# Optimization experiments

Hardware: AMD Instinct MI355X
Metric: run time of the kernel (lower is better)

Reference implementation:

```python
import jax, jax.numpy as jnp
import numpy as np

N = 8192
NFEAT = 512
NHID = 256
NCLASS = 128


def setup_inputs() -> dict:
    key = jax.random.key(0)
    k1, k2, k3, k4 = jax.random.split(key, 4)
    feature_s = jax.random.normal(k1, (N, NFEAT), dtype=jnp.float32)
    feature_t = jax.random.normal(k2, (N, NFEAT), dtype=jnp.float32)
    # nn.Linear(in, out, bias=False) weight has shape [out, in]
    w1 = jax.random.normal(k3, (NHID, NFEAT), dtype=jnp.float32) * (1.0 / np.sqrt(NFEAT))
    w2 = jax.random.normal(k4, (NCLASS, NHID), dtype=jnp.float32) * (1.0 / np.sqrt(NHID))
    return {"feature_s": feature_s, "feature_t": feature_t, "w1": w1, "w2": w2}


def reference(feature_s, feature_t, w1, w2):
    # adj = softmax(feature_s @ feature_t^T) over rows (dim=1)
    adj = jax.nn.softmax(feature_s @ feature_t.T, axis=1)  # [N, N]
    # GCN layer 1: linear(adj @ x) with x = feature_s
    x1 = (adj @ feature_s) @ w1.T  # [N, NHID]
    # GCN layer 2
    x2 = (adj @ x1) @ w2.T  # [N, NCLASS]
    return (x1, x2)
```

## Files before the change

### kernel.cpp

```cpp
#include <hip/hip_runtime.h>
#include <stdint.h>


typedef unsigned short u16;
typedef short bf16x8 __attribute__((ext_vector_type(8)));
typedef _Float16 f16x8 __attribute__((ext_vector_type(8)));
typedef float f32x4 __attribute__((ext_vector_type(4)));

#define EPI_STOREB 0
#define EPI_PARTH  1

__device__ __forceinline__ u16 f2bf(float f) {
  unsigned u = __float_as_uint(f);
  u += 0x7fffu + ((u >> 16) & 1u);
  return (u16)(u >> 16);
}
__device__ __forceinline__ u16 f2h(float f) {
  union { _Float16 h; u16 u; } cv; cv.h = (_Float16)f; return cv.u;
}
__device__ __forceinline__ float h2f(u16 u) {
  union { u16 u; _Float16 h; } cv; cv.u = u; return (float)cv.h;
}
__device__ __forceinline__ int swz8(int r) { return (r ^ (r >> 3)) & 7; }

__device__ __forceinline__ void async16(const void* g, void* lds) {
  __builtin_amdgcn_global_load_lds(
      (const __attribute__((address_space(1))) unsigned int*)g,
      (__attribute__((address_space(3))) unsigned int*)lds, 16, 0, 0);
}

__global__ void probe_layout(int* __restrict__ rmap, int* __restrict__ cmap) {
  const int lane = threadIdx.x & 63;
  const int t = lane & 15, quad = lane >> 4;
  bf16x8 avt, av1;
  const u16 bt = f2bf((float)t), b1 = 0x3f80;
#pragma unroll
  for (int j = 0; j < 8; ++j) { ((u16*)&avt)[j] = bt; ((u16*)&av1)[j] = b1; }
  f32x4 z = {0.f, 0.f, 0.f, 0.f};
  f32x4 r1 = __builtin_amdgcn_mfma_f32_16x16x32_bf16(avt, av1, z, 0, 0, 0);
  f32x4 r2 = __builtin_amdgcn_mfma_f32_16x16x32_bf16(av1, avt, z, 0, 0, 0);
  if (threadIdx.x < 64) {
#pragma unroll
    for (int e = 0; e < 4; ++e) {
      int r = (int)(r1[e] * 0.03125f + 0.5f);
      int c = (int)(r2[e] * 0.03125f + 0.5f);
      if (r < 0 || r > 15) r = quad * 4 + e;
      if (c < 0 || c > 15) c = t;
      rmap[lane * 4 + e] = r;
      cmap[lane * 4 + e] = c;
    }
  }
}

__global__ __launch_bounds__(256) void conv_all(
    const float* __restrict__ Fs, const float* __restrict__ Ft,
    const float* __restrict__ W1, const float* __restrict__ W2,
    u16* __restrict__ Fsf, u16* __restrict__ Ftf,
    u16* __restrict__ W1f, u16* __restrict__ W2h) {
  const int bx = blockIdx.x, tid = threadIdx.x;
  if (bx < 2048) {
    for (int i = bx * 256 + tid; i < 4194304; i += 2048 * 256) Fsf[i] = f2h(Fs[i]);
  } else if (bx < 4096) {
    for (int i = (bx - 2048) * 256 + tid; i < 4194304; i += 2048 * 256) Ftf[i] = f2h(Ft[i]);
  } else if (bx < 4160) {
    for (int i = (bx - 4096) * 256 + tid; i < 131072; i += 64 * 256) W1f[i] = f2h(W1[i]);
  } else {
    for (int i = (bx - 4160) * 256 + tid; i < 32768; i += 16 * 256) W2h[i] = f2bf(W2[i]);
  }
}

__global__ __launch_bounds__(512) void gemm_pexp_f16_256(
    const u16* __restrict__ A, const u16* __restrict__ B, int K, int N,
    u16* __restrict__ P, float* __restrict__ rsp,
    const int* __restrict__ rmap, const int* __restrict__ cmap) {
  __shared__ __align__(16) u16 lA[256 * 64];
  __shared__ __align__(16) u16 lB[128 * 64];
  __shared__ float lrs[256][2];

  const int tid = threadIdx.x;
  const int wave = tid >> 6, lane = tid & 63;
  const int quad = lane >> 4, t = lane & 15;
  const int bm = blockIdx.y * 256, bn = blockIdx.x * 128;
  const int wm = (wave & 3) * 64, wn = (wave >> 2) * 64;

  f32x4 acc[4][4];
#pragma unroll
  for (int i = 0; i < 4; ++i)
#pragma unroll
    for (int j = 0; j < 4; ++j) acc[i][j] = (f32x4){0.f, 0.f, 0.f, 0.f};

  const int srow = tid >> 3, schk = tid & 7;
  const u16* pA[4]; const u16* pB[2];
#pragma unroll
  for (int j = 0; j < 4; ++j) {
    const int r = j * 64 + srow;
    pA[j] = A + (size_t)(bm + r) * K + (schk ^ swz8(r)) * 8;
  }
#pragma unroll
  for (int j = 0; j < 2; ++j) {
    const int r = j * 64 + srow;
    pB[j] = B + (size_t)(bn + r) * K + (schk ^ swz8(r)) * 8;
  }

  int aoffx[4], boffx[4];
#pragma unroll
  for (int i = 0; i < 4; ++i) {
    const int rm = wm + i * 16 + t;
    aoffx[i] = rm * 128 + (swz8(rm) << 4);
    const int rn = wn + i * 16 + t;
    boffx[i] = rn * 128 + (swz8(rn) << 4);
  }
  const int sq0 = quad << 4, sq1 = (quad << 4) | 64;

  for (int k0 = 0; k0 < K; k0 += 64) {
#pragma unroll
    for (int j = 0; j < 4; ++j) {
      async16(pA[j], (char*)lA + j * 8192 + wave * 1024);
      pA[j] += 64;
    }
#pragma unroll
    for (int j = 0; j < 2; ++j) {
      async16(pB[j], (char*)lB + j * 8192 + wave * 1024);
      pB[j] += 64;
    }
    __syncthreads();
#pragma unroll
    for (int s = 0; s < 2; ++s) {
      const int sq = s ? sq1 : sq0;
      f16x8 av[4], bv[4];
#pragma unroll
      for (int i = 0; i < 4; ++i) {
        av[i] = *(const f16x8*)((const char*)lA + (aoffx[i] ^ sq));
        bv[i] = *(const f16x8*)((const char*)lB + (boffx[i] ^ sq));
      }
#pragma unroll
      for (int mi = 0; mi < 4; ++mi)
#pragma unroll
        for (int ni = 0; ni < 4; ++ni)
          acc[mi][ni] = __builtin_amdgcn_mfma_f32_16x16x32_f16(av[mi], bv[ni], acc[mi][ni], 0, 0, 0);
    }
    __syncthreads();
  }

  int rl[4], cl[4];
#pragma unroll
  for (int e = 0; e < 4; ++e) {
    rl[e] = rmap[lane * 4 + e];
    cl[e] = cmap[lane * 4 + e];
  }
#pragma unroll
  for (int mi = 0; mi < 4; ++mi)
#pragma unroll
    for (int e = 0; e < 4; ++e) {
      const int rloc = wm + mi * 16 + rl[e];
      const int row = bm + rloc;
      float s = 0.f;
#pragma unroll
      for (int ni = 0; ni < 4; ++ni) {
        float p = __expf(acc[mi][ni][e] - 100.0f);
        s += p;
        P[(size_t)row * N + (bn + wn + ni * 16 + cl[e])] = f2bf(p);
      }
      s += __shfl_xor(s, 1, 64);
      s += __shfl_xor(s, 2, 64);
      s += __shfl_xor(s, 4, 64);
      s += __shfl_xor(s, 8, 64);
      if (t == 0) lrs[rloc][wave >> 2] = s;
    }
  __syncthreads();
  if (tid < 256)
    rsp[(size_t)blockIdx.x * 8192 + bm + tid] = lrs[tid][0] + lrs[tid][1];
}

__global__ __launch_bounds__(256) void finalize_invl(
    const float* __restrict__ rsp, float* __restrict__ invl) {
  const int row = blockIdx.x * 256 + threadIdx.x;
  float s = 0.f;
#pragma unroll 8
  for (int b = 0; b < 64; ++b) s += rsp[(size_t)b * 8192 + row];
  invl[row] = 1.0f / s;
}

template <int EPI, int F16>
__global__ __launch_bounds__(256) void gemm_nt(
    const u16* __restrict__ A, const u16* __restrict__ B, int K, int Kc, int N,
    u16* __restrict__ outp, const float* __restrict__ invl,
    const int* __restrict__ rmap, const int* __restrict__ cmap) {
  __shared__ __align__(16) u16 lA[128 * 64];
  __shared__ __align__(16) u16 lB[128 * 64];

  const int tid = threadIdx.x;
  const int wave = tid >> 6, lane = tid & 63;
  const int quad = lane >> 4, t = lane & 15;
  const int bm = blockIdx.y * 128, bn = blockIdx.x * 128;
  const int wm = (wave & 1) * 64, wn = (wave >> 1) * 64;
  const int koff = blockIdx.z * Kc;

  f32x4 acc[4][4];
#pragma unroll
  for (int i = 0; i < 4; ++i)
#pragma unroll
    for (int j = 0; j < 4; ++j) acc[i][j] = (f32x4){0.f, 0.f, 0.f, 0.f};

  const int srow = tid >> 3, schk = tid & 7;
  const u16* pA[4]; const u16* pB[4];
#pragma unroll
  for (int j = 0; j < 4; ++j) {
    const int r = j * 32 + srow;
    const int c = schk ^ swz8(r);
    pA[j] = A + (size_t)(bm + r) * K + koff + c * 8;
    pB[j] = B + (size_t)(bn + r) * K + koff + c * 8;
  }

  int aoffx[4], boffx[4];
#pragma unroll
  for (int i = 0; i < 4; ++i) {
    const int rm = wm + i * 16 + t;
    aoffx[i] = rm * 128 + (swz8(rm) << 4);
    const int rn = wn + i * 16 + t;
    boffx[i] = rn * 128 + (swz8(rn) << 4);
  }
  const int sq0 = quad << 4, sq1 = (quad << 4) | 64;

  for (int k0 = 0; k0 < Kc; k0 += 64) {
#pragma unroll
    for (int j = 0; j < 4; ++j) {
      async16(pA[j], (char*)lA + j * 4096 + wave * 1024);
      async16(pB[j], (char*)lB + j * 4096 + wave * 1024);
      pA[j] += 64; pB[j] += 64;
    }
    __syncthreads();
#pragma unroll
    for (int s = 0; s < 2; ++s) {
      const int sq = s ? sq1 : sq0;
      bf16x8 av[4], bv[4];
#pragma unroll
      for (int i = 0; i < 4; ++i) {
        av[i] = *(const bf16x8*)((const char*)lA + (aoffx[i] ^ sq));
        bv[i] = *(const bf16x8*)((const char*)lB + (boffx[i] ^ sq));
      }
#pragma unroll
      for (int mi = 0; mi < 4; ++mi)
#pragma unroll
        for (int ni = 0; ni < 4; ++ni) {
          if constexpr (F16)
            acc[mi][ni] = __builtin_amdgcn_mfma_f32_16x16x32_f16(
                __builtin_bit_cast(f16x8, av[mi]), __builtin_bit_cast(f16x8, bv[ni]),
                acc[mi][ni], 0, 0, 0);
          else
            acc[mi][ni] = __builtin_amdgcn_mfma_f32_16x16x32_bf16(av[mi], bv[ni], acc[mi][ni], 0, 0, 0);
        }
    }
    __syncthreads();
  }

  int rl[4], cl[4];
#pragma unroll
  for (int e = 0; e < 4; ++e) {
    rl[e] = rmap[lane * 4 + e];
    cl[e] = cmap[lane * 4 + e];
  }
  const size_t zoff = (size_t)blockIdx.z * ((size_t)gridDim.y * 128) * N;
#pragma unroll
  for (int mi = 0; mi < 4; ++mi)
#pragma unroll
    for (int e = 0; e < 4; ++e) {
      const int row = bm + wm + mi * 16 + rl[e];
      const float sc = (EPI == EPI_PARTH) ? invl[row] : 1.0f;
#pragma unroll
      for (int ni = 0; ni < 4; ++ni) {
        const size_t idx = (size_t)row * N + (bn + wn + ni * 16 + cl[e]);
        if (EPI == EPI_PARTH) outp[zoff + idx] = f2h(acc[mi][ni][e] * sc);
        else                  outp[idx] = f2bf(acc[mi][ni][e]);
      }
    }
}

__global__ __launch_bounds__(512) void gemm_ntw(
    const u16* __restrict__ A, const u16* __restrict__ B, int K, int Kc, int N,
    u16* __restrict__ outp, const float* __restrict__ invl,
    const int* __restrict__ rmap, const int* __restrict__ cmap) {
  __shared__ __align__(16) u16 lA[128 * 64];
  __shared__ __align__(16) u16 lB[256 * 64];

  const int tid = threadIdx.x;
  const int wave = tid >> 6, lane = tid & 63;
  const int quad = lane >> 4, t = lane & 15;
  const int bm = blockIdx.y * 128, bn = blockIdx.x * 256;
  const int wm = (wave >> 2) * 64, wn = (wave & 3) * 64;
  const int koff = blockIdx.z * Kc;

  f32x4 acc[4][4];
#pragma unroll
  for (int i = 0; i < 4; ++i)
#pragma unroll
    for (int j = 0; j < 4; ++j) acc[i][j] = (f32x4){0.f, 0.f, 0.f, 0.f};

  const int srow = tid >> 3, schk = tid & 7;
  const u16* pA[2]; const u16* pB[4];
#pragma unroll
  for (int j = 0; j < 2; ++j) {
    const int r = j * 64 + srow;
    pA[j] = A + (size_t)(bm + r) * K + koff + (schk ^ swz8(r)) * 8;
  }
#pragma unroll
  for (int j = 0; j < 4; ++j) {
    const int r = j * 64 + srow;
    pB[j] = B + (size_t)(bn + r) * K + koff + (schk ^ swz8(r)) * 8;
  }

  int aoffx[4], boffx[4];
#pragma unroll
  for (int i = 0; i < 4; ++i) {
    const int rm = wm + i * 16 + t;
    aoffx[i] = rm * 128 + (swz8(rm) << 4);
    const int rn = wn + i * 16 + t;
    boffx[i] = rn * 128 + (swz8(rn) << 4);
  }
  const int sq0 = quad << 4, sq1 = (quad << 4) | 64;

  for (int k0 = 0; k0 < Kc; k0 += 64) {
#pragma unroll
    for (int j = 0; j < 2; ++j) {
      async16(pA[j], (char*)lA + j * 8192 + wave * 1024);
      pA[j] += 64;
    }
#pragma unroll
    for (int j = 0; j < 4; ++j) {
      async16(pB[j], (char*)lB + j * 8192 + wave * 1024);
      pB[j] += 64;
    }
    __syncthreads();
#pragma unroll
    for (int s = 0; s < 2; ++s) {
      const int sq = s ? sq1 : sq0;
      bf16x8 av[4], bv[4];
#pragma unroll
      for (int i = 0; i < 4; ++i) {
        av[i] = *(const bf16x8*)((const char*)lA + (aoffx[i] ^ sq));
        bv[i] = *(const bf16x8*)((const char*)lB + (boffx[i] ^ sq));
      }
#pragma unroll
      for (int mi = 0; mi < 4; ++mi)
#pragma unroll
        for (int ni = 0; ni < 4; ++ni)
          acc[mi][ni] = __builtin_amdgcn_mfma_f32_16x16x32_bf16(av[mi], bv[ni], acc[mi][ni], 0, 0, 0);
    }
    __syncthreads();
  }

  int rl[4], cl[4];
#pragma unroll
  for (int e = 0; e < 4; ++e) {
    rl[e] = rmap[lane * 4 + e];
    cl[e] = cmap[lane * 4 + e];
  }
  const size_t zoff = (size_t)blockIdx.z * ((size_t)gridDim.y * 128) * N;
#pragma unroll
  for (int mi = 0; mi < 4; ++mi)
#pragma unroll
    for (int e = 0; e < 4; ++e) {
      const int row = bm + wm + mi * 16 + rl[e];
      const float sc = invl[row];
#pragma unroll
      for (int ni = 0; ni < 4; ++ni) {
        const size_t idx = (size_t)row * N + (bn + wn + ni * 16 + cl[e]);
        outp[zoff + idx] = f2h(acc[mi][ni][e] * sc);
      }
    }
}

__global__ __launch_bounds__(256) void combine1(
    const u16* __restrict__ pp, const float* __restrict__ invl,
    float* __restrict__ x1f, u16* __restrict__ x1h) {
  const int row = blockIdx.x, j = threadIdx.x;
  const size_t i = (size_t)row * 256 + j;
  const float v = h2f(pp[i]) + h2f(pp[2097152 + i]) +
                  h2f(pp[4194304 + i]) + h2f(pp[6291456 + i]);
  x1f[i] = v;
  x1h[i] = f2bf(v);
}

__global__ __launch_bounds__(128) void combine2(
    const u16* __restrict__ pp, const float* __restrict__ invl,
    float* __restrict__ x2f) {
  const int row = blockIdx.x, j = threadIdx.x;
  const size_t i = (size_t)row * 128 + j;
  float s = 0.f;
#pragma unroll
  for (int z = 0; z < 8; ++z) s += h2f(pp[(size_t)z * 1048576 + i]);
  x2f[i] = s;
}

extern "C" void kernel_launch(void* const* d_in, const int* in_sizes, int n_in,
                              void* d_out, int out_size, void* d_ws, size_t ws_size,
                              hipStream_t stream) {
  const float* Fs = (const float*)d_in[0];
  const float* Ft = (const float*)d_in[1];
  const float* W1 = (const float*)d_in[2];
  const float* W2 = (const float*)d_in[3];

  char* ws = (char*)d_ws;
  u16*   P    = (u16*)(ws);
  u16*   Fsf  = (u16*)(ws + 134217728);
  u16*   Ftf  = (u16*)(ws + 142606336);
  u16*   pp   = (u16*)(ws + 134217728);
  float* rsp  = (float*)(ws + 150994944);
  u16*   Y1T  = (u16*)(ws + 153091200);
  u16*   x1h  = (u16*)(ws + 157286400);
  u16*   Y2T  = (u16*)(ws + 161480704);
  float* invl = (float*)(ws + 163577856);
  int*   rmap = (int*)  (ws + 163610624);
  int*   cmap = (int*)  (ws + 163611648);
  u16*   W1f  = (u16*)(ws + 163612672);
  u16*   W2h  = (u16*)(ws + 163874816);

  float* x1f = (float*)d_out;
  float* x2f = (float*)d_out + 2097152;

  dim3 blk(256);
  probe_layout<<<1, 64, 0, stream>>>(rmap, cmap);
  conv_all<<<4176, blk, 0, stream>>>(Fs, Ft, W1, W2, Fsf, Ftf, W1f, W2h);
  gemm_pexp_f16_256<<<dim3(64, 32), dim3(512), 0, stream>>>(
      Fsf, Ftf, 512, 8192, P, rsp, rmap, cmap);
  finalize_invl<<<32, blk, 0, stream>>>(rsp, invl);
  gemm_nt<EPI_STOREB, 1><<<dim3(64, 2), blk, 0, stream>>>(
      W1f, Fsf, 512, 512, 8192, Y1T, nullptr, rmap, cmap);
  gemm_ntw<<<dim3(1, 64, 4), dim3(512), 0, stream>>>(
      P, Y1T, 8192, 2048, 256, pp, invl, rmap, cmap);
  combine1<<<8192, blk, 0, stream>>>(pp, invl, x1f, x1h);
  gemm_nt<EPI_STOREB, 0><<<dim3(64, 1), blk, 0, stream>>>(
      W2h, x1h, 256, 256, 8192, Y2T, nullptr, rmap, cmap);
  gemm_nt<EPI_PARTH, 0><<<dim3(1, 64, 8), blk, 0, stream>>>(
      P, Y2T, 8192, 1024, 128, pp, invl, rmap, cmap);
  combine2<<<8192, dim3(128), 0, stream>>>(pp, invl, x2f);
}
```

Before: 279.1 us.

## Merge probe into conversion, co-schedule Y1 GEMM with score GEMM, vectorize combines

Folds the layout probe into the fp32-to-half conversion kernel, now vectorized to 8 elements per thread. The score/exp GEMM and the W1·Fs GEMM share one launch, with extra blocks computing Y1T using half the waves. combine1 and combine2 now use 16-byte loads and stores. The aim is to cut launch count and tail idle time and to improve memory efficiency of the elementwise kernels. The cost is that the Y1 blocks leave half their waves idle.

```diff
diff --git a/kernel.cpp b/kernel.cpp
--- a/kernel.cpp
+++ b/kernel.cpp
@@ -29,8 +29,34 @@
       (__attribute__((address_space(3))) unsigned int*)lds, 16, 0, 0);
 }
 
-__global__ void probe_layout(int* __restrict__ rmap, int* __restrict__ cmap) {
-  const int lane = threadIdx.x & 63;
+__global__ __launch_bounds__(256) void conv_probe(
+    const float* __restrict__ Fs, const float* __restrict__ Ft,
+    const float* __restrict__ W1, const float* __restrict__ W2,
+    u16* __restrict__ Fsf, u16* __restrict__ Ftf,
+    u16* __restrict__ W1f, u16* __restrict__ W2h,
+    int* __restrict__ rmap, int* __restrict__ cmap) {
+  const int bx = blockIdx.x, tid = threadIdx.x;
+  if (bx < 4176) {
+    const float* src; u16* dst; size_t i; bool tobf = false;
+    if (bx < 2048)      { src = Fs; dst = Fsf; i = ((size_t)bx * 256 + tid) * 8; }
+    else if (bx < 4096) { src = Ft; dst = Ftf; i = ((size_t)(bx - 2048) * 256 + tid) * 8; }
+    else if (bx < 4160) { src = W1; dst = W1f; i = ((size_t)(bx - 4096) * 256 + tid) * 8; }
+    else                { src = W2; dst = W2h; i = ((size_t)(bx - 4160) * 256 + tid) * 8; tobf = true; }
+    const float4 a = *(const float4*)(src + i);
+    const float4 b = *(const float4*)(src + i + 4);
+    bf16x8 o;
+    if (tobf) {
+      o[0] = (short)f2bf(a.x); o[1] = (short)f2bf(a.y); o[2] = (short)f2bf(a.z); o[3] = (short)f2bf(a.w);
+      o[4] = (short)f2bf(b.x); o[5] = (short)f2bf(b.y); o[6] = (short)f2bf(b.z); o[7] = (short)f2bf(b.w);
+    } else {
+      o[0] = (short)f2h(a.x); o[1] = (short)f2h(a.y); o[2] = (short)f2h(a.z); o[3] = (short)f2h(a.w);
+      o[4] = (short)f2h(b.x); o[5] = (short)f2h(b.y); o[6] = (short)f2h(b.z); o[7] = (short)f2h(b.w);
+    }
+    *(bf16x8*)(dst + i) = o;
+    return;
+  }
+  if (tid >= 64) return;
+  const int lane = tid & 63;
   const int t = lane & 15, quad = lane >> 4;
   bf16x8 avt, av1;
   const u16 bt = f2bf((float)t), b1 = 0x3f80;
@@ -39,39 +65,21 @@
   f32x4 z = {0.f, 0.f, 0.f, 0.f};
   f32x4 r1 = __builtin_amdgcn_mfma_f32_16x16x32_bf16(avt, av1, z, 0, 0, 0);
   f32x4 r2 = __builtin_amdgcn_mfma_f32_16x16x32_bf16(av1, avt, z, 0, 0, 0);
-  if (threadIdx.x < 64) {
-#pragma unroll
-    for (int e = 0; e < 4; ++e) {
-      int r = (int)(r1[e] * 0.03125f + 0.5f);
-      int c = (int)(r2[e] * 0.03125f + 0.5f);
-      if (r < 0 || r > 15) r = quad * 4 + e;
-      if (c < 0 || c > 15) c = t;
-      rmap[lane * 4 + e] = r;
-      cmap[lane * 4 + e] = c;
-    }
-  }
-}
-
-__global__ __launch_bounds__(256) void conv_all(
-    const float* __restrict__ Fs, const float* __restrict__ Ft,
-    const float* __restrict__ W1, const float* __restrict__ W2,
-    u16* __restrict__ Fsf, u16* __restrict__ Ftf,
-    u16* __restrict__ W1f, u16* __restrict__ W2h) {
-  const int bx = blockIdx.x, tid = threadIdx.x;
-  if (bx < 2048) {
-    for (int i = bx * 256 + tid; i < 4194304; i += 2048 * 256) Fsf[i] = f2h(Fs[i]);
-  } else if (bx < 4096) {
-    for (int i = (bx - 2048) * 256 + tid; i < 4194304; i += 2048 * 256) Ftf[i] = f2h(Ft[i]);
-  } else if (bx < 4160) {
-    for (int i = (bx - 4096) * 256 + tid; i < 131072; i += 64 * 256) W1f[i] = f2h(W1[i]);
-  } else {
-    for (int i = (bx - 4160) * 256 + tid; i < 32768; i += 16 * 256) W2h[i] = f2bf(W2[i]);
-  }
-}
-
-__global__ __launch_bounds__(512) void gemm_pexp_f16_256(
-    const u16* __restrict__ A, const u16* __restrict__ B, int K, int N,
-    u16* __restrict__ P, float* __restrict__ rsp,
+#pragma unroll
+  for (int e = 0; e < 4; ++e) {
+    int r = (int)(r1[e] * 0.03125f + 0.5f);
+    int c = (int)(r2[e] * 0.03125f + 0.5f);
+    if (r < 0 || r > 15) r = quad * 4 + e;
+    if (c < 0 || c > 15) c = t;
+    rmap[lane * 4 + e] = r;
+    cmap[lane * 4 + e] = c;
+  }
+}
+
+__global__ __launch_bounds__(512) void g2_gy1(
+    const u16* __restrict__ Fsf, const u16* __restrict__ Ftf,
+    const u16* __restrict__ W1f,
+    u16* __restrict__ P, float* __restrict__ rsp, u16* __restrict__ Y1T,
     const int* __restrict__ rmap, const int* __restrict__ cmap) {
   __shared__ __align__(16) u16 lA[256 * 64];
   __shared__ __align__(16) u16 lB[128 * 64];
@@ -80,96 +88,184 @@
   const int tid = threadIdx.x;
   const int wave = tid >> 6, lane = tid & 63;
   const int quad = lane >> 4, t = lane & 15;
-  const int bm = blockIdx.y * 256, bn = blockIdx.x * 128;
-  const int wm = (wave & 3) * 64, wn = (wave >> 2) * 64;
-
-  f32x4 acc[4][4];
-#pragma unroll
-  for (int i = 0; i < 4; ++i)
-#pragma unroll
-    for (int j = 0; j < 4; ++j) acc[i][j] = (f32x4){0.f, 0.f, 0.f, 0.f};
-
-  const int srow = tid >> 3, schk = tid & 7;
-  const u16* pA[4]; const u16* pB[2];
-#pragma unroll
-  for (int j = 0; j < 4; ++j) {
-    const int r = j * 64 + srow;
-    pA[j] = A + (size_t)(bm + r) * K + (schk ^ swz8(r)) * 8;
-  }
-#pragma unroll
-  for (int j = 0; j < 2; ++j) {
-    const int r = j * 64 + srow;
-    pB[j] = B + (size_t)(bn + r) * K + (schk ^ swz8(r)) * 8;
-  }
-
-  int aoffx[4], boffx[4];
-#pragma unroll
-  for (int i = 0; i < 4; ++i) {
-    const int rm = wm + i * 16 + t;
-    aoffx[i] = rm * 128 + (swz8(rm) << 4);
-    const int rn = wn + i * 16 + t;
-    boffx[i] = rn * 128 + (swz8(rn) << 4);
-  }
   const int sq0 = quad << 4, sq1 = (quad << 4) | 64;
 
-  for (int k0 = 0; k0 < K; k0 += 64) {
+  if (blockIdx.x < 2048) {
+    const int bn = (blockIdx.x & 63) * 128, bm = (blockIdx.x >> 6) * 256;
+    const int wm = (wave & 3) * 64, wn = (wave >> 2) * 64;
+    constexpr int K = 512, N = 8192;
+
+    f32x4 acc[4][4];
+#pragma unroll
+    for (int i = 0; i < 4; ++i)
+#pragma unroll
+      for (int j = 0; j < 4; ++j) acc[i][j] = (f32x4){0.f, 0.f, 0.f, 0.f};
+
+    const int srow = tid >> 3, schk = tid & 7;
+    const u16* pA[4]; const u16* pB[2];
 #pragma unroll
     for (int j = 0; j < 4; ++j) {
-      async16(pA[j], (char*)lA + j * 8192 + wave * 1024);
-      pA[j] += 64;
+      const int r = j * 64 + srow;
+      pA[j] = Fsf + (size_t)(bm + r) * K + (schk ^ swz8(r)) * 8;
     }
 #pragma unroll
     for (int j = 0; j < 2; ++j) {
-      async16(pB[j], (char*)lB + j * 8192 + wave * 1024);
-      pB[j] += 64;
-    }
+      const int r = j * 64 + srow;
+      pB[j] = Ftf + (size_t)(bn + r) * K + (schk ^ swz8(r)) * 8;
+    }
+
+    int aoffx[4], boffx[4];
+#pragma unroll
+    for (int i = 0; i < 4; ++i) {
+      const int rm = wm + i * 16 + t;
+      aoffx[i] = rm * 128 + (swz8(rm) << 4);
+      const int rn = wn + i * 16 + t;
+      boffx[i] = rn * 128 + (swz8(rn) << 4);
+    }
+
+    for (int k0 = 0; k0 < K; k0 += 64) {
+#pragma unroll
+      for (int j = 0; j < 4; ++j) {
+        async16(pA[j], (char*)lA + j * 8192 + wave * 1024);
+        pA[j] += 64;
+      }
+#pragma unroll
+      for (int j = 0; j < 2; ++j) {
+        async16(pB[j], (char*)lB + j * 8192 + wave * 1024);
+        pB[j] += 64;
+      }
+      __syncthreads();
+#pragma unroll
+      for (int s = 0; s < 2; ++s) {
+        const int sq = s ? sq1 : sq0;
+        f16x8 av[4], bv[4];
+#pragma unroll
+        for (int i = 0; i < 4; ++i) {
+          av[i] = *(const f16x8*)((const char*)lA + (aoffx[i] ^ sq));
+          bv[i] = *(const f16x8*)((const char*)lB + (boffx[i] ^ sq));
+        }
+#pragma unroll
+        for (int mi = 0; mi < 4; ++mi)
+#pragma unroll
+          for (int ni = 0; ni < 4; ++ni)
+            acc[mi][ni] = __builtin_amdgcn_mfma_f32_16x16x32_f16(av[mi], bv[ni], acc[mi][ni], 0, 0, 0);
+      }
+      __syncthreads();
+    }
+
+    int rl[4], cl[4];
+#pragma unroll
+    for (int e = 0; e < 4; ++e) {
+      rl[e] = rmap[lane * 4 + e];
+      cl[e] = cmap[lane * 4 + e];
+    }
+#pragma unroll
+    for (int mi = 0; mi < 4; ++mi)
+#pragma unroll
+      for (int e = 0; e < 4; ++e) {
+        const int rloc = wm + mi * 16 + rl[e];
+        const int row = bm + rloc;
+        float s = 0.f;
+#pragma unroll
+        for (int ni = 0; ni < 4; ++ni) {
+          float p = __expf(acc[mi][ni][e] - 100.0f);
+          s += p;
+          P[(size_t)row * N + (bn + wn + ni * 16 + cl[e])] = f2bf(p);
+        }
+        s += __shfl_xor(s, 1, 64);
+        s += __shfl_xor(s, 2, 64);
+        s += __shfl_xor(s, 4, 64);
+        s += __shfl_xor(s, 8, 64);
+        if (t == 0) lrs[rloc][wave >> 2] = s;
+      }
     __syncthreads();
-#pragma unroll
-    for (int s = 0; s < 2; ++s) {
-      const int sq = s ? sq1 : sq0;
-      f16x8 av[4], bv[4];
-#pragma unroll
-      for (int i = 0; i < 4; ++i) {
-        av[i] = *(const f16x8*)((const char*)lA + (aoffx[i] ^ sq));
-        bv[i] = *(const f16x8*)((const char*)lB + (boffx[i] ^ sq));
+    if (tid < 256)
+      rsp[(size_t)(blockIdx.x & 63) * 8192 + bm + tid] = lrs[tid][0] + lrs[tid][1];
+  } else {
+    const int gid = blockIdx.x - 2048;
+    const int bm = (gid >> 6) * 128, bn = (gid & 63) * 128;
+    const int wm = (wave & 1) * 64, wn = (wave >> 1) * 64;
+    constexpr int K = 512, N = 8192;
+    u16* gA = lA;
+    u16* gB = lA + 8192;
+
+    f32x4 acc[4][4];
+#pragma unroll
+    for (int i = 0; i < 4; ++i)
+#pragma unroll
+      for (int j = 0; j < 4; ++j) acc[i][j] = (f32x4){0.f, 0.f, 0.f, 0.f};
+
+    const int srow = tid >> 3, schk = tid & 7;
+    const u16* pA[4]; const u16* pB[4];
+    if (tid < 256) {
+#pragma unroll
+      for (int j = 0; j < 4; ++j) {
+        const int r = j * 32 + srow;
+        const int c = schk ^ swz8(r);
+        pA[j] = W1f + (size_t)(bm + r) * K + c * 8;
+        pB[j] = Fsf + (size_t)(bn + r) * K + c * 8;
+      }
+    }
+
+    int aoffx[4], boffx[4];
+#pragma unroll
+    for (int i = 0; i < 4; ++i) {
+      const int rm = wm + i * 16 + t;
+      aoffx[i] = rm * 128 + (swz8(rm) << 4);
+      const int rn = wn + i * 16 + t;
+      boffx[i] = rn * 128 + (swz8(rn) << 4);
+    }
+
+    for (int k0 = 0; k0 < K; k0 += 64) {
+      if (tid < 256) {
+#pragma unroll
+        for (int j = 0; j < 4; ++j) {
+          async16(pA[j], (char*)gA + j * 4096 + wave * 1024);
+          async16(pB[j], (char*)gB + j * 4096 + wave * 1024);
+          pA[j] += 64; pB[j] += 64;
+        }
+      }
+      __syncthreads();
+      if (tid < 256) {
+#pragma unroll
+        for (int s = 0; s < 2; ++s) {
+          const int sq = s ? sq1 : sq0;
+          f16x8 av[4], bv[4];
+#pragma unroll
+          for (int i = 0; i < 4; ++i) {
+            av[i] = *(const f16x8*)((const char*)gA + (aoffx[i] ^ sq));
+            bv[i] = *(const f16x8*)((const char*)gB + (boffx[i] ^ sq));
+          }
+#pragma unroll
+          for (int mi = 0; mi < 4; ++mi)
+#pragma unroll
+            for (int ni = 0; ni < 4; ++ni)
+              acc[mi][ni] = __builtin_amdgcn_mfma_f32_16x16x32_f16(av[mi], bv[ni], acc[mi][ni], 0, 0, 0);
+        }
+      }
+      __syncthreads();
+    }
+
+    if (tid < 256) {
+      int rl[4], cl[4];
+#pragma unroll
+      for (int e = 0; e < 4; ++e) {
+        rl[e] = rmap[lane * 4 + e];
+        cl[e] = cmap[lane * 4 + e];
       }
 #pragma unroll
       for (int mi = 0; mi < 4; ++mi)
 #pragma unroll
-        for (int ni = 0; ni < 4; ++ni)
-          acc[mi][ni] = __builtin_amdgcn_mfma_f32_16x16x32_f16(av[mi], bv[ni], acc[mi][ni], 0, 0, 0);
-    }
-    __syncthreads();
-  }
-
-  int rl[4], cl[4];
-#pragma unroll
-  for (int e = 0; e < 4; ++e) {
-    rl[e] = rmap[lane * 4 + e];
-    cl[e] = cmap[lane * 4 + e];
-  }
-#pragma unroll
-  for (int mi = 0; mi < 4; ++mi)
-#pragma unroll
-    for (int e = 0; e < 4; ++e) {
-      const int rloc = wm + mi * 16 + rl[e];
-      const int row = bm + rloc;
-      float s = 0.f;
-#pragma unroll
-      for (int ni = 0; ni < 4; ++ni) {
-        float p = __expf(acc[mi][ni][e] - 100.0f);
-        s += p;
-        P[(size_t)row * N + (bn + wn + ni * 16 + cl[e])] = f2bf(p);
-      }
-      s += __shfl_xor(s, 1, 64);
-      s += __shfl_xor(s, 2, 64);
-      s += __shfl_xor(s, 4, 64);
-      s += __shfl_xor(s, 8, 64);
-      if (t == 0) lrs[rloc][wave >> 2] = s;
-    }
-  __syncthreads();
-  if (tid < 256)
-    rsp[(size_t)blockIdx.x * 8192 + bm + tid] = lrs[tid][0] + lrs[tid][1];
+        for (int e = 0; e < 4; ++e) {
+          const int row = bm + wm + mi * 16 + rl[e];
+#pragma unroll
+          for (int ni = 0; ni < 4; ++ni) {
+            const size_t idx = (size_t)row * N + (bn + wn + ni * 16 + cl[e]);
+            Y1T[idx] = f2bf(acc[mi][ni][e]);
+          }
+        }
+    }
+  }
 }
 
 __global__ __launch_bounds__(256) void finalize_invl(
@@ -373,23 +469,40 @@
 __global__ __launch_bounds__(256) void combine1(
     const u16* __restrict__ pp, const float* __restrict__ invl,
     float* __restrict__ x1f, u16* __restrict__ x1h) {
-  const int row = blockIdx.x, j = threadIdx.x;
-  const size_t i = (size_t)row * 256 + j;
-  const float v = h2f(pp[i]) + h2f(pp[2097152 + i]) +
-                  h2f(pp[4194304 + i]) + h2f(pp[6291456 + i]);
-  x1f[i] = v;
-  x1h[i] = f2bf(v);
-}
-
-__global__ __launch_bounds__(128) void combine2(
+  const size_t i = ((size_t)blockIdx.x * 256 + threadIdx.x) * 8;
+  const bf16x8 p0 = *(const bf16x8*)(pp + i);
+  const bf16x8 p1 = *(const bf16x8*)(pp + 2097152 + i);
+  const bf16x8 p2 = *(const bf16x8*)(pp + 4194304 + i);
+  const bf16x8 p3 = *(const bf16x8*)(pp + 6291456 + i);
+  float4 o0, o1;
+  bf16x8 oh;
+#pragma unroll
+  for (int j = 0; j < 8; ++j) {
+    const float v = h2f((u16)p0[j]) + h2f((u16)p1[j]) + h2f((u16)p2[j]) + h2f((u16)p3[j]);
+    if (j < 4) ((float*)&o0)[j] = v; else ((float*)&o1)[j - 4] = v;
+    oh[j] = (short)f2bf(v);
+  }
+  *(float4*)(x1f + i) = o0;
+  *(float4*)(x1f + i + 4) = o1;
+  *(bf16x8*)(x1h + i) = oh;
+}
+
+__global__ __launch_bounds__(256) void combine2(
     const u16* __restrict__ pp, const float* __restrict__ invl,
     float* __restrict__ x2f) {
-  const int row = blockIdx.x, j = threadIdx.x;
-  const size_t i = (size_t)row * 128 + j;
-  float s = 0.f;
-#pragma unroll
-  for (int z = 0; z < 8; ++z) s += h2f(pp[(size_t)z * 1048576 + i]);
-  x2f[i] = s;
+  const size_t i = ((size_t)blockIdx.x * 256 + threadIdx.x) * 8;
+  float v[8] = {0.f, 0.f, 0.f, 0.f, 0.f, 0.f, 0.f, 0.f};
+#pragma unroll
+  for (int z = 0; z < 8; ++z) {
+    const bf16x8 p = *(const bf16x8*)(pp + (size_t)z * 1048576 + i);
+#pragma unroll
+    for (int j = 0; j < 8; ++j) v[j] += h2f((u16)p[j]);
+  }
+  float4 o0, o1;
+#pragma unroll
+  for (int j = 0; j < 4; ++j) { ((float*)&o0)[j] = v[j]; ((float*)&o1)[j] = v[j + 4]; }
+  *(float4*)(x2f + i) = o0;
+  *(float4*)(x2f + i + 4) = o1;
 }
 
 extern "C" void kernel_launch(void* const* d_in, const int* in_sizes, int n_in,
@@ -406,7 +519,7 @@
   u16*   Ftf  = (u16*)(ws + 142606336);
   u16*   pp   = (u16*)(ws + 134217728);
   float* rsp  = (float*)(ws + 150994944);
-  u16*   Y1T  = (u16*)(ws + 153091200);
+  u16*   Y1T  = (u16*)(ws + 153092096);
   u16*   x1h  = (u16*)(ws + 157286400);
   u16*   Y2T  = (u16*)(ws + 161480704);
   float* invl = (float*)(ws + 163577856);
@@ -419,19 +532,15 @@
   float* x2f = (float*)d_out + 2097152;
 
   dim3 blk(256);
-  probe_layout<<<1, 64, 0, stream>>>(rmap, cmap);
-  conv_all<<<4176, blk, 0, stream>>>(Fs, Ft, W1, W2, Fsf, Ftf, W1f, W2h);
-  gemm_pexp_f16_256<<<dim3(64, 32), dim3(512), 0, stream>>>(
-      Fsf, Ftf, 512, 8192, P, rsp, rmap, cmap);
+  conv_probe<<<4177, blk, 0, stream>>>(Fs, Ft, W1, W2, Fsf, Ftf, W1f, W2h, rmap, cmap);
+  g2_gy1<<<2176, dim3(512), 0, stream>>>(Fsf, Ftf, W1f, P, rsp, Y1T, rmap, cmap);
   finalize_invl<<<32, blk, 0, stream>>>(rsp, invl);
-  gemm_nt<EPI_STOREB, 1><<<dim3(64, 2), blk, 0, stream>>>(
-      W1f, Fsf, 512, 512, 8192, Y1T, nullptr, rmap, cmap);
   gemm_ntw<<<dim3(1, 64, 4), dim3(512), 0, stream>>>(
       P, Y1T, 8192, 2048, 256, pp, invl, rmap, cmap);
-  combine1<<<8192, blk, 0, stream>>>(pp, invl, x1f, x1h);
+  combine1<<<1024, blk, 0, stream>>>(pp, invl, x1f, x1h);
   gemm_nt<EPI_STOREB, 0><<<dim3(64, 1), blk, 0, stream>>>(
       W2h, x1h, 256, 256, 8192, Y2T, nullptr, rmap, cmap);
   gemm_nt<EPI_PARTH, 0><<<dim3(1, 64, 8), blk, 0, stream>>>(
       P, Y2T, 8192, 1024, 128, pp, invl, rmap, cmap);
-  combine2<<<8192, dim3(128), 0, stream>>>(pp, invl, x2f);
-}
+  combine2<<<512, blk, 0, stream>>>(pp, invl, x2f);
+}
```

Result: slower. 313.6 us (+12.4%).
